# Kernel tuning notes

Measured on AMD Instinct MI355X. Metric: run time of the kernel, lower is better.

The kernel has to match this reference:

```python
import jax, jax.numpy as jnp
import numpy as np

DG = 8   # deformable groups
KK = 9   # 3x3 kernel positions


def conv3x3(x, w, b):
    # x: [B,C,H,W], w: [O,I,3,3] -> SAME conv, stride 1
    y = jax.lax.conv_general_dilated(x, w, (1, 1), 'SAME',
                                     dimension_numbers=('NCHW', 'OIHW', 'NCHW'))
    return y + b[None, :, None, None]


def modulated_deform_conv(x, offset, mask, w, b):
    # x: [B,C,H,W]; offset: [B,DG,KK,2,H,W] (dy,dx per group/kernel-pos);
    # mask: [B,DG,KK,H,W]; w: [O,C,3,3]; groups=1, stride=1, pad=1, dil=1.
    B, C, H, W = x.shape
    cg = C // DG  # channels per deformable group
    dy = offset[:, :, :, 0]  # [B,DG,KK,H,W]
    dx = offset[:, :, :, 1]
    ky, kx = jnp.meshgrid(jnp.arange(3), jnp.arange(3), indexing='ij')
    ky = (ky.reshape(KK) - 1).astype(x.dtype)  # kernel y offsets (pad=1)
    kx = (kx.reshape(KK) - 1).astype(x.dtype)
    py = dy + jnp.arange(H, dtype=x.dtype).reshape(1, 1, 1, H, 1) + ky.reshape(1, 1, KK, 1, 1)
    px = dx + jnp.arange(W, dtype=x.dtype).reshape(1, 1, 1, 1, W) + kx.reshape(1, 1, KK, 1, 1)
    y0 = jnp.floor(py)
    x0 = jnp.floor(px)
    ly = py - y0  # bilinear fractions
    lx = px - x0
    y0i = y0.astype(jnp.int32)
    x0i = x0.astype(jnp.int32)
    xf = x.reshape(B, DG, cg, H * W)

    def gather(yi, xi):
        # zero padding outside the image (per-corner validity)
        valid = ((yi >= 0) & (yi < H) & (xi >= 0) & (xi < W)).astype(x.dtype)
        idx = jnp.clip(yi, 0, H - 1) * W + jnp.clip(xi, 0, W - 1)  # [B,DG,KK,H,W]
        g = jnp.take_along_axis(xf, idx.reshape(B, DG, 1, KK * H * W), axis=-1)
        return g.reshape(B, DG, cg, KK, H, W) * valid[:, :, None]

    v = (((1 - ly) * (1 - lx))[:, :, None] * gather(y0i, x0i)
         + ((1 - ly) * lx)[:, :, None] * gather(y0i, x0i + 1)
         + (ly * (1 - lx))[:, :, None] * gather(y0i + 1, x0i)
         + (ly * lx)[:, :, None] * gather(y0i + 1, x0i + 1))
    v = (v * mask[:, :, None]).reshape(B, C, KK, H, W)  # modulated im2col
    out = jnp.einsum('bckhw,ock->bohw', v, w.reshape(w.shape[0], C, KK))
    return out + b[None, :, None, None]


def setup_inputs() -> dict:
    key = jax.random.key(0)
    ks = jax.random.split(key, 6)
    B, C, H, W = 8, 64, 128, 128
    f = lambda k, s: jax.random.normal(k, s, dtype=jnp.float32)
    return {
        'cat_fea': f(ks[0], (B, C, H, W)),
        'f_fea': f(ks[1], (B, C, H, W)),
        'w_off2d': f(ks[2], (C, C, 3, 3)) * 0.05,
        'b_off2d': jnp.zeros((C,), jnp.float32),
        'w_coff': f(ks[3], (3 * DG * KK, C, 3, 3)) * 0.01,  # small => near-zero offsets, as in DCNv2Pack init
        'b_coff': jnp.zeros((3 * DG * KK,), jnp.float32),
        'w_dconv': f(ks[4], (C, C, 3, 3)) * 0.05,
        'b_dconv': jnp.zeros((C,), jnp.float32),
    }


def reference(cat_fea, f_fea, w_off2d, b_off2d, w_coff, b_coff, w_dconv, b_dconv):
    # offset1 = self.off2d_1(cat_fea)
    offset_feat = conv3x3(cat_fea, w_off2d, b_off2d)
    # DCNv2Pack: conv_offset on the extra feature, chunk into o1,o2,mask
    off = conv3x3(offset_feat, w_coff, b_coff)  # [B, 3*DG*KK, H, W]
    o1, o2, m = jnp.split(off, 3, axis=1)
    B, _, H, W = off.shape
    # offset = cat(o1,o2); CUDA kernel reads channel ((g*KK+i)*2 + {0:y,1:x})
    offset = jnp.concatenate([o1, o2], axis=1).reshape(B, DG, KK, 2, H, W)
    mask = jax.nn.sigmoid(m).reshape(B, DG, KK, H, W)
    return modulated_deform_conv(f_fea, offset, mask, w_dconv, b_dconv)
```

## Files before the change

### kernel.cpp

```cpp
#include <hip/hip_runtime.h>
#include <math.h>

typedef __attribute__((ext_vector_type(4))) float f32x4;
typedef __attribute__((ext_vector_type(8))) short bf16x8;

#define HH 128
#define WW 128
#define HWSZ 16384
#define BHW 131072
#define BB 8

__device__ __forceinline__ float bf2f(ushort u) {
    union { uint i; float f; } x; x.i = ((uint)u) << 16; return x.f;
}
__device__ __forceinline__ ushort f2bf(float f) {
    union { float f; uint i; } x; x.f = f;
    uint r = (x.i + 0x7fffu + ((x.i >> 16) & 1u)) >> 16;
    return (ushort)r;
}

__global__ __launch_bounds__(256) void to_gp_bf16(const float* __restrict__ x,
                                                  ushort* __restrict__ y) {
    __shared__ ushort lds[64][66];
    int blk = blockIdx.x;
    int b = blk >> 8;
    int hw0 = (blk & 255) << 6;
    int t = threadIdx.x;
    int lane = t & 63;
    int q = t >> 6;
#pragma unroll
    for (int i = 0; i < 16; i++) {
        int c = i * 4 + q;
        lds[c][lane] = f2bf(x[((size_t)(b * 64 + c) << 14) + hw0 + lane]);
    }
    __syncthreads();
#pragma unroll
    for (int it = 0; it < 2; it++) {
        int id = it * 256 + t;
        int cg = id >> 6;
        int px = id & 63;
        uint pk[4];
#pragma unroll
        for (int j = 0; j < 4; j++)
            pk[j] = (uint)lds[cg * 8 + 2 * j][px] | ((uint)lds[cg * 8 + 2 * j + 1][px] << 16);
        *(uint4*)(y + ((((size_t)b * 8 + cg) << 14) + hw0 + px) * 8) = *(uint4*)pk;
    }
}

__global__ __launch_bounds__(256) void prep_wa(const float* __restrict__ w,
                                               ushort* __restrict__ wa, int Co, int Co_pad) {
    int idx = blockIdx.x * 256 + threadIdx.x;
    if (idx >= Co_pad * 576) return;
    int co = idx / 576, r = idx % 576;
    int kk = r >> 6, ci = r & 63;
    ushort v = 0;
    if (co < Co) v = f2bf(w[(co * 64 + ci) * 9 + kk]);
    wa[idx] = v;
}

template<int NCO, int MODE>
__global__ __launch_bounds__(256, 3) void conv_gemm2_k(
    const ushort* __restrict__ xt, const ushort* __restrict__ wa,
    const float* __restrict__ bias, ushort* __restrict__ y,
    uint* __restrict__ dyxp, ushort* __restrict__ mpl, int Cout) {
    __shared__ ushort Al[NCO * 64 * 64];
    __shared__ ushort Bt[64 * 64];
    int t = threadIdx.x;
    int orig = blockIdx.x;
    int blk = (orig & 7) * 256 + (orig >> 3);
    int b = blk >> 8;
    int h = (blk >> 1) & 127;
    int w0 = (blk & 1) << 6;
    int lane = t & 63;
    int wv = t >> 6;
    int lg = lane >> 4;
    int lr = lane & 15;
    int rs = (lr & 7) << 4;
    int asw = ((lane & 7) ^ (lane >> 3)) << 4;
    const char* wab = (const char*)wa;

    f32x4 acc[NCO][4];
#pragma unroll
    for (int n = 0; n < NCO; n++)
#pragma unroll
        for (int j = 0; j < 4; j++) acc[n][j] = f32x4{0, 0, 0, 0};

#pragma unroll 1
    for (int kk = 0; kk < 9; kk++) {
        int ky = kk / 3;
        int kx = kk - ky * 3;
        __syncthreads();
#pragma unroll
        for (int a = 0; a < 2 * NCO; a++) {
            int rb = wv * (NCO * 16) + a * 8;
            const char* g = wab + (size_t)(rb + (lane >> 3)) * 1152 + kk * 128 + asw;
            __builtin_amdgcn_global_load_lds(
                (const __attribute__((address_space(1))) void*)g,
                (__attribute__((address_space(3))) void*)((char*)Al + rb * 128),
                16, 0, 0);
        }
        int hy = h + ky - 1;
        int wx = w0 + lane + kx - 1;
        bool val = ((unsigned)hy < 128u) && ((unsigned)wx < 128u);
        uint4 v0 = {0u, 0u, 0u, 0u}, v1 = {0u, 0u, 0u, 0u};
        if (val) {
            const ushort* gb = xt + ((((size_t)b * 8 + wv) << 14) + (hy << 7) + wx) * 8;
            v0 = *(const uint4*)gb;
            v1 = *(const uint4*)(gb + (4ull << 17));
        }
        int swl = (lane & 7) << 4;
        *(uint4*)((char*)Bt + lane * 128 + ((wv * 16) ^ swl)) = v0;
        *(uint4*)((char*)Bt + lane * 128 + (((wv + 4) * 16) ^ swl)) = v1;
        __syncthreads();
#pragma unroll
        for (int n = 0; n < NCO; n++) {
            int ar = n * 64 + wv * 16 + lr;
            bf16x8 a0 = *(const bf16x8*)((char*)Al + ar * 128 + ((lg * 16) ^ rs));
            bf16x8 a1 = *(const bf16x8*)((char*)Al + ar * 128 + ((lg * 16 + 64) ^ rs));
#pragma unroll
            for (int j = 0; j < 4; j++) {
                int pr = j * 16 + lr;
                bf16x8 b0 = *(const bf16x8*)((char*)Bt + pr * 128 + ((lg * 16) ^ rs));
                bf16x8 b1 = *(const bf16x8*)((char*)Bt + pr * 128 + ((lg * 16 + 64) ^ rs));
                acc[n][j] = __builtin_amdgcn_mfma_f32_16x16x32_bf16(a0, b0, acc[n][j], 0, 0, 0);
                acc[n][j] = __builtin_amdgcn_mfma_f32_16x16x32_bf16(a1, b1, acc[n][j], 0, 0, 0);
            }
        }
    }

#pragma unroll
    for (int n = 0; n < NCO; n++) {
        int co_g = n * 64 + wv * 16 + lg * 4;
        if (co_g < Cout) {
            float bs[4];
#pragma unroll
            for (int r = 0; r < 4; r++) bs[r] = bias[co_g + r];
#pragma unroll
            for (int j = 0; j < 4; j++) {
                int pxl = j * 16 + lr;
                int hw = (h << 7) + w0 + pxl;
                int bhw = (b << 14) + hw;
                if (MODE == 0) {
                    int cg = co_g >> 3, cs = co_g & 7;
                    uint2 s2;
                    s2.x = (uint)f2bf(acc[n][j][0] + bs[0]) | ((uint)f2bf(acc[n][j][1] + bs[1]) << 16);
                    s2.y = (uint)f2bf(acc[n][j][2] + bs[2]) | ((uint)f2bf(acc[n][j][3] + bs[3]) << 16);
                    *(uint2*)(y + ((((size_t)b * 8 + cg) << 14) + hw) * 8 + cs) = s2;
                } else if (co_g < 144) {
                    int p0 = co_g >> 1;
                    uint u0 = (uint)f2bf(acc[n][j][0] + bs[0]) | ((uint)f2bf(acc[n][j][1] + bs[1]) << 16);
                    uint u1 = (uint)f2bf(acc[n][j][2] + bs[2]) | ((uint)f2bf(acc[n][j][3] + bs[3]) << 16);
                    dyxp[(size_t)p0 * BHW + bhw] = u0;
                    dyxp[(size_t)(p0 + 1) * BHW + bhw] = u1;
                } else {
#pragma unroll
                    for (int r = 0; r < 4; r++) {
                        float f = 1.f / (1.f + __expf(-(acc[n][j][r] + bs[r])));
                        mpl[(size_t)(co_g - 144 + r) * BHW + bhw] = f2bf(f);
                    }
                }
            }
        }
    }
}

__global__ __launch_bounds__(256, 4) void deform_reg_k(
    const ushort* __restrict__ xg, const uint* __restrict__ dyxp,
    const ushort* __restrict__ mpl, const ushort* __restrict__ wa,
    const float* __restrict__ bias, float* __restrict__ out) {
    int t = threadIdx.x;
    int orig = blockIdx.x;
    int blk = (orig & 7) * 256 + (orig >> 3);
    int b = blk >> 8;
    int h = (blk >> 1) & 127;
    int w0 = (blk & 1) << 6;
    int lane = t & 63;
    int wv = t >> 6;
    int lg = lane >> 4;
    int lr = lane & 15;
    int wabs = w0 + wv * 16 + lr;
    int bhw = (b << 14) + (h << 7) + wabs;

    f32x4 acc[4] = {f32x4{0,0,0,0}, f32x4{0,0,0,0}, f32x4{0,0,0,0}, f32x4{0,0,0,0}};

#pragma unroll
    for (int c = 0; c < 18; c++) {
        const int dg_l = ((c & 1) << 2);
        const int tap = c >> 1;
        const int ky = tap / 3;
        const int kx = tap - ky * 3;
        int dg = dg_l + lg;
        int p = dg * 9 + tap;
        uint dyx = dyxp[(size_t)p * BHW + bhw];
        float m = bf2f(mpl[(size_t)p * BHW + bhw]);
        float dy = bf2f((ushort)(dyx & 0xffff));
        float dx = bf2f((ushort)(dyx >> 16));
        float py = dy + (float)(h + ky - 1);
        float px_ = dx + (float)(wabs + kx - 1);
        float fy = floorf(py), fx = floorf(px_);
        int y0 = (int)fy, x0 = (int)fx;
        int y1 = y0 + 1, x1 = x0 + 1;
        float ly = py - fy, lx = px_ - fx;
        bool vy0 = (unsigned)y0 < (unsigned)HH, vy1 = (unsigned)y1 < (unsigned)HH;
        bool vx0 = (unsigned)x0 < (unsigned)WW, vx1 = (unsigned)x1 < (unsigned)WW;
        float w00 = (vy0 && vx0) ? (1.f - ly) * (1.f - lx) * m : 0.f;
        float w01 = (vy0 && vx1) ? (1.f - ly) * lx * m : 0.f;
        float w10 = (vy1 && vx0) ? ly * (1.f - lx) * m : 0.f;
        float w11 = (vy1 && vx1) ? ly * lx * m : 0.f;
        int y0c = min(max(y0, 0), HH - 1), y1c = min(max(y1, 0), HH - 1);
        int x0c = min(max(x0, 0), WW - 1), x1c = min(max(x1, 0), WW - 1);
        const ushort* gb = xg + (((size_t)b * 8 + dg) << 17);
        uint4 q00 = *(const uint4*)(gb + ((y0c << 7) + x0c) * 8);
        uint4 q01 = *(const uint4*)(gb + ((y0c << 7) + x1c) * 8);
        uint4 q10 = *(const uint4*)(gb + ((y1c << 7) + x0c) * 8);
        uint4 q11 = *(const uint4*)(gb + ((y1c << 7) + x1c) * 8);
        const ushort* u00 = (const ushort*)&q00;
        const ushort* u01 = (const ushort*)&q01;
        const ushort* u10 = (const ushort*)&q10;
        const ushort* u11 = (const ushort*)&q11;
        uint pk[4];
#pragma unroll
        for (int c2 = 0; c2 < 4; c2++) {
            float v0 = w00 * bf2f(u00[2*c2])   + w01 * bf2f(u01[2*c2])
                     + w10 * bf2f(u10[2*c2])   + w11 * bf2f(u11[2*c2]);
            float v1 = w00 * bf2f(u00[2*c2+1]) + w01 * bf2f(u01[2*c2+1])
                     + w10 * bf2f(u10[2*c2+1]) + w11 * bf2f(u11[2*c2+1]);
            pk[c2] = (uint)f2bf(v0) | ((uint)f2bf(v1) << 16);
        }
        bf16x8 bfrag = *(bf16x8*)pk;
        const ushort* wac = wa + c * 32 + lg * 8;
#pragma unroll
        for (int n = 0; n < 4; n++) {
            bf16x8 a = *(const bf16x8*)(wac + (size_t)(n * 16 + lr) * 576);
            acc[n] = __builtin_amdgcn_mfma_f32_16x16x32_bf16(a, bfrag, acc[n], 0, 0, 0);
        }
    }

    int hw = (h << 7) + wabs;
#pragma unroll
    for (int n = 0; n < 4; n++) {
        int co_g = n * 16 + lg * 4;
#pragma unroll
        for (int r = 0; r < 4; r++) {
            out[((size_t)(b * 64 + co_g + r) << 14) + hw] = acc[n][r] + bias[co_g + r];
        }
    }
}

extern "C" void kernel_launch(void* const* d_in, const int* in_sizes, int n_in,
                              void* d_out, int out_size, void* d_ws, size_t ws_size,
                              hipStream_t stream) {
    const float* cat_fea = (const float*)d_in[0];
    const float* f_fea   = (const float*)d_in[1];
    const float* w_off2d = (const float*)d_in[2];
    const float* b_off2d = (const float*)d_in[3];
    const float* w_coff  = (const float*)d_in[4];
    const float* b_coff  = (const float*)d_in[5];
    const float* w_dconv = (const float*)d_in[6];
    const float* b_dconv = (const float*)d_in[7];
    float* out = (float*)d_out;

    ushort* x1t      = (ushort*)d_ws;
    ushort* xft      = x1t + 8388608;
    ushort* off_feat = xft + 8388608;
    uint*   dyxp     = (uint*)(off_feat + 8388608);
    ushort* mpl      = (ushort*)(dyxp + 9437184);
    ushort* wa1      = mpl + 9437184;
    ushort* wa2      = wa1 + 36864;
    ushort* wad      = wa2 + 147456;

    to_gp_bf16<<<2048, 256, 0, stream>>>(cat_fea, x1t);
    to_gp_bf16<<<2048, 256, 0, stream>>>(f_fea, xft);
    prep_wa<<<(64 * 576 + 255) / 256, 256, 0, stream>>>(w_off2d, wa1, 64, 64);
    prep_wa<<<(256 * 576 + 255) / 256, 256, 0, stream>>>(w_coff, wa2, 216, 256);
    prep_wa<<<(64 * 576 + 255) / 256, 256, 0, stream>>>(w_dconv, wad, 64, 64);

    conv_gemm2_k<1, 0><<<2048, 256, 0, stream>>>(x1t, wa1, b_off2d, off_feat,
                                                 nullptr, nullptr, 64);
    conv_gemm2_k<4, 1><<<2048, 256, 0, stream>>>(off_feat, wa2, b_coff, nullptr,
                                                 dyxp, mpl, 216);
    deform_reg_k<<<2048, 256, 0, stream>>>(xft, dyxp, mpl, wad, b_dconv, out);
}
```

Before: 188.4 us.

## Software-pipeline deform gather loop with double-buffered corner and weight loads

The deformable conv kernel now preloads all 18 packed offset words into registers up front. It also double-buffers the bilinear corner gathers, interpolation weights and MFMA A-fragments, so the loads for step c+1 are issued before the math and MFMAs for step c. This aims to hide global gather latency behind compute. The cost is much higher register pressure, so the occupancy hint is lowered from 4 to 3 waves per SIMD.

Result: no change. 187.7 us (-0.4%).

```diff
diff --git a/kernel.cpp b/kernel.cpp
--- a/kernel.cpp
+++ b/kernel.cpp
@@ -164,7 +164,7 @@
     }
 }
 
-__global__ __launch_bounds__(256, 4) void deform_reg_k(
+__global__ __launch_bounds__(256, 3) void deform_reg2_k(
     const ushort* __restrict__ xg, const uint* __restrict__ dyxp,
     const ushort* __restrict__ mpl, const ushort* __restrict__ wa,
     const float* __restrict__ bias, float* __restrict__ out) {
@@ -181,60 +181,88 @@
     int wabs = w0 + wv * 16 + lr;
     int bhw = (b << 14) + (h << 7) + wabs;
 
+    uint dyxv[18];
+#pragma unroll
+    for (int c = 0; c < 18; c++) {
+        int dg = ((c & 1) << 2) + lg;
+        int tap = c >> 1;
+        dyxv[c] = dyxp[(size_t)(dg * 9 + tap) * BHW + bhw];
+    }
+
+    uint4 qg[2][4];
+    f32x4 wt4[2];
+    bf16x8 afr[2][4];
     f32x4 acc[4] = {f32x4{0,0,0,0}, f32x4{0,0,0,0}, f32x4{0,0,0,0}, f32x4{0,0,0,0}};
 
+#define DPRE(c) do {                                                            \
+    const int tap = (c) >> 1;                                                   \
+    const int ky = tap / 3;                                                     \
+    const int kx = tap - ky * 3;                                                \
+    int dg = (((c) & 1) << 2) + lg;                                             \
+    float m = bf2f(mpl[(size_t)(dg * 9 + tap) * BHW + bhw]);                    \
+    uint dyx = dyxv[(c)];                                                       \
+    float dy = bf2f((ushort)(dyx & 0xffff));                                    \
+    float dx = bf2f((ushort)(dyx >> 16));                                       \
+    float py = dy + (float)(h + ky - 1);                                        \
+    float px_ = dx + (float)(wabs + kx - 1);                                    \
+    float fy = floorf(py), fx = floorf(px_);                                    \
+    int y0 = (int)fy, x0 = (int)fx;                                             \
+    int y1 = y0 + 1, x1 = x0 + 1;                                               \
+    float ly = py - fy, lx = px_ - fx;                                          \
+    bool vy0 = (unsigned)y0 < 128u, vy1 = (unsigned)y1 < 128u;                  \
+    bool vx0 = (unsigned)x0 < 128u, vx1 = (unsigned)x1 < 128u;                  \
+    f32x4 wv4;                                                                  \
+    wv4[0] = (vy0 && vx0) ? (1.f - ly) * (1.f - lx) * m : 0.f;                  \
+    wv4[1] = (vy0 && vx1) ? (1.f - ly) * lx * m : 0.f;                          \
+    wv4[2] = (vy1 && vx0) ? ly * (1.f - lx) * m : 0.f;                          \
+    wv4[3] = (vy1 && vx1) ? ly * lx * m : 0.f;                                  \
+    wt4[(c) & 1] = wv4;                                                         \
+    int y0c = min(max(y0, 0), 127), y1c = min(max(y1, 0), 127);                 \
+    int x0c = min(max(x0, 0), 127), x1c = min(max(x1, 0), 127);                 \
+    const ushort* gb = xg + (((size_t)b * 8 + dg) << 17);                       \
+    qg[(c) & 1][0] = *(const uint4*)(gb + ((y0c << 7) + x0c) * 8);              \
+    qg[(c) & 1][1] = *(const uint4*)(gb + ((y0c << 7) + x1c) * 8);              \
+    qg[(c) & 1][2] = *(const uint4*)(gb + ((y1c << 7) + x0c) * 8);              \
+    qg[(c) & 1][3] = *(const uint4*)(gb + ((y1c << 7) + x1c) * 8);              \
+} while (0)
+
+#define APRE(c) do {                                                            \
+    const ushort* wac = wa + (c) * 32 + lg * 8;                                 \
+    _Pragma("unroll")                                                           \
+    for (int n = 0; n < 4; n++)                                                 \
+        afr[(c) & 1][n] = *(const bf16x8*)(wac + (size_t)(n * 16 + lr) * 576);  \
+} while (0)
+
+    DPRE(0);
+    APRE(0);
+
 #pragma unroll
     for (int c = 0; c < 18; c++) {
-        const int dg_l = ((c & 1) << 2);
-        const int tap = c >> 1;
-        const int ky = tap / 3;
-        const int kx = tap - ky * 3;
-        int dg = dg_l + lg;
-        int p = dg * 9 + tap;
-        uint dyx = dyxp[(size_t)p * BHW + bhw];
-        float m = bf2f(mpl[(size_t)p * BHW + bhw]);
-        float dy = bf2f((ushort)(dyx & 0xffff));
-        float dx = bf2f((ushort)(dyx >> 16));
-        float py = dy + (float)(h + ky - 1);
-        float px_ = dx + (float)(wabs + kx - 1);
-        float fy = floorf(py), fx = floorf(px_);
-        int y0 = (int)fy, x0 = (int)fx;
-        int y1 = y0 + 1, x1 = x0 + 1;
-        float ly = py - fy, lx = px_ - fx;
-        bool vy0 = (unsigned)y0 < (unsigned)HH, vy1 = (unsigned)y1 < (unsigned)HH;
-        bool vx0 = (unsigned)x0 < (unsigned)WW, vx1 = (unsigned)x1 < (unsigned)WW;
-        float w00 = (vy0 && vx0) ? (1.f - ly) * (1.f - lx) * m : 0.f;
-        float w01 = (vy0 && vx1) ? (1.f - ly) * lx * m : 0.f;
-        float w10 = (vy1 && vx0) ? ly * (1.f - lx) * m : 0.f;
-        float w11 = (vy1 && vx1) ? ly * lx * m : 0.f;
-        int y0c = min(max(y0, 0), HH - 1), y1c = min(max(y1, 0), HH - 1);
-        int x0c = min(max(x0, 0), WW - 1), x1c = min(max(x1, 0), WW - 1);
-        const ushort* gb = xg + (((size_t)b * 8 + dg) << 17);
-        uint4 q00 = *(const uint4*)(gb + ((y0c << 7) + x0c) * 8);
-        uint4 q01 = *(const uint4*)(gb + ((y0c << 7) + x1c) * 8);
-        uint4 q10 = *(const uint4*)(gb + ((y1c << 7) + x0c) * 8);
-        uint4 q11 = *(const uint4*)(gb + ((y1c << 7) + x1c) * 8);
-        const ushort* u00 = (const ushort*)&q00;
-        const ushort* u01 = (const ushort*)&q01;
-        const ushort* u10 = (const ushort*)&q10;
-        const ushort* u11 = (const ushort*)&q11;
+        if (c < 17) {
+            DPRE(c + 1);
+            APRE(c + 1);
+        }
+        f32x4 wc = wt4[c & 1];
+        const ushort* u00 = (const ushort*)&qg[c & 1][0];
+        const ushort* u01 = (const ushort*)&qg[c & 1][1];
+        const ushort* u10 = (const ushort*)&qg[c & 1][2];
+        const ushort* u11 = (const ushort*)&qg[c & 1][3];
         uint pk[4];
 #pragma unroll
         for (int c2 = 0; c2 < 4; c2++) {
-            float v0 = w00 * bf2f(u00[2*c2])   + w01 * bf2f(u01[2*c2])
-                     + w10 * bf2f(u10[2*c2])   + w11 * bf2f(u11[2*c2]);
-            float v1 = w00 * bf2f(u00[2*c2+1]) + w01 * bf2f(u01[2*c2+1])
-                     + w10 * bf2f(u10[2*c2+1]) + w11 * bf2f(u11[2*c2+1]);
+            float v0 = wc[0] * bf2f(u00[2*c2])   + wc[1] * bf2f(u01[2*c2])
+                     + wc[2] * bf2f(u10[2*c2])   + wc[3] * bf2f(u11[2*c2]);
+            float v1 = wc[0] * bf2f(u00[2*c2+1]) + wc[1] * bf2f(u01[2*c2+1])
+                     + wc[2] * bf2f(u10[2*c2+1]) + wc[3] * bf2f(u11[2*c2+1]);
             pk[c2] = (uint)f2bf(v0) | ((uint)f2bf(v1) << 16);
         }
         bf16x8 bfrag = *(bf16x8*)pk;
-        const ushort* wac = wa + c * 32 + lg * 8;
-#pragma unroll
-        for (int n = 0; n < 4; n++) {
-            bf16x8 a = *(const bf16x8*)(wac + (size_t)(n * 16 + lr) * 576);
-            acc[n] = __builtin_amdgcn_mfma_f32_16x16x32_bf16(a, bfrag, acc[n], 0, 0, 0);
-        }
-    }
+#pragma unroll
+        for (int n = 0; n < 4; n++)
+            acc[n] = __builtin_amdgcn_mfma_f32_16x16x32_bf16(afr[c & 1][n], bfrag, acc[n], 0, 0, 0);
+    }
+#undef DPRE
+#undef APRE
 
     int hw = (h << 7) + wabs;
 #pragma unroll
@@ -279,5 +307,5 @@
                                                  nullptr, nullptr, 64);
     conv_gemm2_k<4, 1><<<2048, 256, 0, stream>>>(off_feat, wa2, b_coff, nullptr,
                                                  dyxp, mpl, 216);
-    deform_reg_k<<<2048, 256, 0, stream>>>(xft, dyxp, mpl, wad, b_dconv, out);
-}
+    deform_reg2_k<<<2048, 256, 0, stream>>>(xft, dyxp, mpl, wad, b_dconv, out);
+}
```
